# Kernel optimization log

Measured on AMD Instinct MI355X. Metric: run time of the kernel, lower is better.

Reference implementation:

```python
import jax, jax.numpy as jnp
import numpy as np

B, L, H, E = 4, 2048, 16, 64
S, D = L, E

def setup_inputs() -> dict:
    key = jax.random.key(0)
    kq, kk, kv = jax.random.split(key, 3)
    queries = jax.random.normal(kq, (B, L, H, E), dtype=jnp.float32)
    keys = jax.random.normal(kk, (B, S, H, E), dtype=jnp.float32)
    values = jax.random.normal(kv, (B, S, H, D), dtype=jnp.float32)
    return {"queries": queries, "keys": keys, "values": values}

def reference(queries, keys, values):
    # FullAttention(mask_flag=True, scale=None, output_attention=False), eval mode (dropout off)
    Bq, Lq, Hq, Eq = queries.shape
    scale = 1.0 / jnp.sqrt(jnp.asarray(Eq, dtype=queries.dtype))
    scores = jnp.einsum('blhe,bshe->bhls', queries, keys)  # [B,H,L,S]
    causal = jnp.triu(jnp.ones((Lq, Lq), dtype=bool), k=1)  # True above diagonal
    neg_inf = jnp.finfo(scores.dtype).min
    scores = jnp.where(causal[None, None, :, :], neg_inf, scores)
    A = jax.nn.softmax(scale * scores, axis=-1)
    V = jnp.einsum('bhls,bshd->blhd', A, values)  # [B,L,H,D]
    return V
```

## Files before the change

kernel.cpp:

```cpp
#include <hip/hip_runtime.h>

typedef _Float16 half8  __attribute__((ext_vector_type(8)));
typedef _Float16 half4v __attribute__((ext_vector_type(4)));
typedef __fp16   pk2    __attribute__((ext_vector_type(2)));
typedef float    f32x16 __attribute__((ext_vector_type(16)));

constexpr int CL = 2048, CH = 16, CE = 64;
constexpr int RS = CH * CE;

union H8 { half8 v; pk2 h[4]; unsigned u[4]; };
union H4 { half4v v; pk2 h[2]; };
union H2 { pk2 h; unsigned u; };

__device__ __forceinline__ int swz(int r) { return ((r ^ (r >> 3)) & 7) << 3; }

__global__ __launch_bounds__(256, 3)
void attn32(const float* __restrict__ Q, const float* __restrict__ K,
            const float* __restrict__ V, float* __restrict__ O) {
  __shared__ _Float16 KS[2][64 * 64];
  __shared__ _Float16 VT[2][64 * 64];

  const int tid = threadIdx.x;
  const int w  = tid >> 6, l = tid & 63;
  const int hi = l >> 5,  ql = l & 31;

  const int bid = blockIdx.x;
  const int bh  = bid & 63;
  const int qt  = 15 - (bid >> 6);
  const int b = bh >> 4, h = bh & 15;
  const int qg0 = qt * 128 + w * 32;
  const int qg  = qg0 + ql;

  const float* qptr = Q + ((size_t)(b * CL + qg) * CH + h) * CE;
  const float qs = 0.125f * 1.44269504089f;
  half8 qf[4];
#pragma unroll
  for (int c = 0; c < 4; ++c) {
    const float4 x0 = *(const float4*)(qptr + c * 16 + hi * 8);
    const float4 x1 = *(const float4*)(qptr + c * 16 + hi * 8 + 4);
    H8 t;
    t.h[0] = __builtin_amdgcn_cvt_pkrtz(x0.x * qs, x0.y * qs);
    t.h[1] = __builtin_amdgcn_cvt_pkrtz(x0.z * qs, x0.w * qs);
    t.h[2] = __builtin_amdgcn_cvt_pkrtz(x1.x * qs, x1.y * qs);
    t.h[3] = __builtin_amdgcn_cvt_pkrtz(x1.z * qs, x1.w * qs);
    qf[c] = t.v;
  }

  f32x16 acc0, acc1;
#pragma unroll
  for (int i = 0; i < 16; ++i) { acc0[i] = 0.f; acc1[i] = 0.f; }
  float m_ = -1e30f, l_ = 0.f;

  const float* Kb = K + ((size_t)b * CL * CH + h) * CE;
  const float* Vb = V + ((size_t)b * CL * CH + h) * CE;

  const int r0 = tid >> 4;
  const int c4 = tid & 15;

  const int ktmax  = 2 * qt + 1;
  const int ktlast = 2 * qt + (w >> 1);

  auto stage_write = [&](int buf, int i, const float4& kx, const float4& vx) {
    const int row = i * 16 + r0;
    H4 t;
    t.h[0] = __builtin_amdgcn_cvt_pkrtz(kx.x, kx.y);
    t.h[1] = __builtin_amdgcn_cvt_pkrtz(kx.z, kx.w);
    *(half4v*)&KS[buf][row * 64 + ((c4 * 4) ^ swz(row))] = t.v;
    VT[buf][(c4 * 4 + 0) * 64 + (row ^ swz(c4 * 4 + 0))] = (_Float16)vx.x;
    VT[buf][(c4 * 4 + 1) * 64 + (row ^ swz(c4 * 4 + 1))] = (_Float16)vx.y;
    VT[buf][(c4 * 4 + 2) * 64 + (row ^ swz(c4 * 4 + 2))] = (_Float16)vx.z;
    VT[buf][(c4 * 4 + 3) * 64 + (row ^ swz(c4 * 4 + 3))] = (_Float16)vx.w;
  };

#pragma unroll
  for (int i = 0; i < 4; ++i) {
    const int row = i * 16 + r0;
    const float4 kx = *(const float4*)(Kb + (size_t)row * RS + c4 * 4);
    const float4 vx = *(const float4*)(Vb + (size_t)row * RS + c4 * 4);
    stage_write(0, i, kx, vx);
  }

  for (int kt = 0; kt <= ktmax; ++kt) {
    const int cur = kt & 1, nxt = cur ^ 1;
    __syncthreads();

    float4 kst[4], vst[4];
    const bool doStage = (kt < ktmax);
    if (doStage) {
      const int kb1 = (kt + 1) * 64;
#pragma unroll
      for (int i = 0; i < 4; ++i) {
        const int row = kb1 + i * 16 + r0;
        kst[i] = *(const float4*)(Kb + (size_t)row * RS + c4 * 4);
        vst[i] = *(const float4*)(Vb + (size_t)row * RS + c4 * 4);
      }
    }

    if (kt <= ktlast) {
      const int kb = kt * 64;
      const bool do1 = (qg0 + 31) >= (kb + 32);

      f32x16 st0, st1;
#pragma unroll
      for (int i = 0; i < 16; ++i) { st0[i] = 0.f; st1[i] = 0.f; }
#pragma unroll
      for (int c = 0; c < 4; ++c) {
        const half8 ka = *(const half8*)&KS[cur][ql * 64 + ((c * 16 + hi * 8) ^ swz(ql))];
        st0 = __builtin_amdgcn_mfma_f32_32x32x16_f16(ka, qf[c], st0, 0, 0, 0);
      }
      if (do1) {
#pragma unroll
        for (int c = 0; c < 4; ++c) {
          const int row = 32 + ql;
          const half8 ka = *(const half8*)&KS[cur][row * 64 + ((c * 16 + hi * 8) ^ swz(row))];
          st1 = __builtin_amdgcn_mfma_f32_32x32x16_f16(ka, qf[c], st1, 0, 0, 0);
        }
      }

      if (kt == ktlast) {
#pragma unroll
        for (int r = 0; r < 16; ++r) {
          const int ko = (r & 3) + 8 * (r >> 2) + 4 * hi;
          if (kb + ko > qg) st0[r] = -1e30f;
          if (kb + 32 + ko > qg) st1[r] = -1e30f;
        }
      }

      float mt;
      {
        float a = fmaxf(fmaxf(fmaxf(st0[0], st0[1]), fmaxf(st0[2], st0[3])),
                        fmaxf(fmaxf(st0[4], st0[5]), fmaxf(st0[6], st0[7])));
        float bm = fmaxf(fmaxf(fmaxf(st0[8], st0[9]), fmaxf(st0[10], st0[11])),
                         fmaxf(fmaxf(st0[12], st0[13]), fmaxf(st0[14], st0[15])));
        mt = fmaxf(a, bm);
        if (do1) {
          float c2 = fmaxf(fmaxf(fmaxf(st1[0], st1[1]), fmaxf(st1[2], st1[3])),
                           fmaxf(fmaxf(st1[4], st1[5]), fmaxf(st1[6], st1[7])));
          float d2 = fmaxf(fmaxf(fmaxf(st1[8], st1[9]), fmaxf(st1[10], st1[11])),
                           fmaxf(fmaxf(st1[12], st1[13]), fmaxf(st1[14], st1[15])));
          mt = fmaxf(mt, fmaxf(c2, d2));
        }
      }
      mt = fmaxf(mt, __shfl_xor(mt, 32));
      const float mn = fmaxf(m_, mt);
      const float corr = exp2f(m_ - mn);
      m_ = mn;

      float rs = 0.f;
#pragma unroll
      for (int r = 0; r < 16; ++r) { st0[r] = exp2f(st0[r] - mn); rs += st0[r]; }
      if (do1) {
#pragma unroll
        for (int r = 0; r < 16; ++r) { st1[r] = exp2f(st1[r] - mn); rs += st1[r]; }
      }
      rs += __shfl_xor(rs, 32);
      l_ = l_ * corr + rs;
#pragma unroll
      for (int r = 0; r < 16; ++r) { acc0[r] *= corr; acc1[r] *= corr; }

      unsigned W0[8], W1[8];
#pragma unroll
      for (int m = 0; m < 8; ++m) {
        H2 u; u.h = __builtin_amdgcn_cvt_pkrtz(st0[2 * m], st0[2 * m + 1]);
        W0[m] = u.u;
      }
      if (do1) {
#pragma unroll
        for (int m = 0; m < 8; ++m) {
          H2 u; u.h = __builtin_amdgcn_cvt_pkrtz(st1[2 * m], st1[2 * m + 1]);
          W1[m] = u.u;
        }
      }

#pragma unroll
      for (int c2 = 0; c2 < 2; ++c2) {
        const unsigned s0 = (unsigned)__shfl_xor((int)W0[4 * c2 + 0], 32);
        const unsigned s1 = (unsigned)__shfl_xor((int)W0[4 * c2 + 1], 32);
        const unsigned s2 = (unsigned)__shfl_xor((int)W0[4 * c2 + 2], 32);
        const unsigned s3 = (unsigned)__shfl_xor((int)W0[4 * c2 + 3], 32);
        H8 f;
        f.u[0] = hi ? s2 : W0[4 * c2 + 0];
        f.u[1] = hi ? s3 : W0[4 * c2 + 1];
        f.u[2] = hi ? W0[4 * c2 + 2] : s0;
        f.u[3] = hi ? W0[4 * c2 + 3] : s1;
        const int kx = c2 * 16 + hi * 8;
        const int d0 = ql, d1 = 32 + ql;
        const half8 va0 = *(const half8*)&VT[cur][d0 * 64 + (kx ^ swz(d0))];
        const half8 va1 = *(const half8*)&VT[cur][d1 * 64 + (kx ^ swz(d1))];
        acc0 = __builtin_amdgcn_mfma_f32_32x32x16_f16(va0, f.v, acc0, 0, 0, 0);
        acc1 = __builtin_amdgcn_mfma_f32_32x32x16_f16(va1, f.v, acc1, 0, 0, 0);
      }
      if (do1) {
#pragma unroll
        for (int c2 = 0; c2 < 2; ++c2) {
          const unsigned s0 = (unsigned)__shfl_xor((int)W1[4 * c2 + 0], 32);
          const unsigned s1 = (unsigned)__shfl_xor((int)W1[4 * c2 + 1], 32);
          const unsigned s2 = (unsigned)__shfl_xor((int)W1[4 * c2 + 2], 32);
          const unsigned s3 = (unsigned)__shfl_xor((int)W1[4 * c2 + 3], 32);
          H8 f;
          f.u[0] = hi ? s2 : W1[4 * c2 + 0];
          f.u[1] = hi ? s3 : W1[4 * c2 + 1];
          f.u[2] = hi ? W1[4 * c2 + 2] : s0;
          f.u[3] = hi ? W1[4 * c2 + 3] : s1;
          const int kx = (2 + c2) * 16 + hi * 8;
          const int d0 = ql, d1 = 32 + ql;
          const half8 va0 = *(const half8*)&VT[cur][d0 * 64 + (kx ^ swz(d0))];
          const half8 va1 = *(const half8*)&VT[cur][d1 * 64 + (kx ^ swz(d1))];
          acc0 = __builtin_amdgcn_mfma_f32_32x32x16_f16(va0, f.v, acc0, 0, 0, 0);
          acc1 = __builtin_amdgcn_mfma_f32_32x32x16_f16(va1, f.v, acc1, 0, 0, 0);
        }
      }
    }

    if (doStage) {
#pragma unroll
      for (int i = 0; i < 4; ++i) stage_write(nxt, i, kst[i], vst[i]);
    }
  }

  const float inv = 1.0f / l_;
  float* obase = O + ((size_t)(b * CL + qg) * CH + h) * CE;
#pragma unroll
  for (int rq = 0; rq < 4; ++rq) {
    float4 o;
    o.x = acc0[4 * rq + 0] * inv; o.y = acc0[4 * rq + 1] * inv;
    o.z = acc0[4 * rq + 2] * inv; o.w = acc0[4 * rq + 3] * inv;
    *(float4*)(obase + rq * 8 + hi * 4) = o;
  }
#pragma unroll
  for (int rq = 0; rq < 4; ++rq) {
    float4 o;
    o.x = acc1[4 * rq + 0] * inv; o.y = acc1[4 * rq + 1] * inv;
    o.z = acc1[4 * rq + 2] * inv; o.w = acc1[4 * rq + 3] * inv;
    *(float4*)(obase + 32 + rq * 8 + hi * 4) = o;
  }
}

extern "C" void kernel_launch(void* const* d_in, const int* in_sizes, int n_in,
                              void* d_out, int out_size, void* d_ws, size_t ws_size,
                              hipStream_t stream) {
  const float* Q = (const float*)d_in[0];
  const float* K = (const float*)d_in[1];
  const float* V = (const float*)d_in[2];
  float* O = (float*)d_out;
  (void)d_ws; (void)ws_size; (void)in_sizes; (void)n_in; (void)out_size;
  attn32<<<dim3(16 * 64), dim3(256), 0, stream>>>(Q, K, V, O);
}
```

Measured before the change: 232.8 us.

## Use 512-thread blocks over 256 query rows with lazy rescale and setprio

Doubles the block to 8 waves covering 256 query rows, so each staged K/V tile is shared by twice as many queries and global K/V traffic drops. The grid is halved and reordered so heavy causal tiles come first. The online-softmax rescale now runs only when the running max grows by more than a threshold, and MFMA sections are wrapped in s_setprio. The key loop is unrolled by two with fixed buffer indices. Risks include lower occupancy, fewer blocks for load balance, and fp16 overflow headroom from the lazy max.

```diff
diff --git a/kernel.cpp b/kernel.cpp
--- a/kernel.cpp
+++ b/kernel.cpp
@@ -14,9 +14,9 @@
 
 __device__ __forceinline__ int swz(int r) { return ((r ^ (r >> 3)) & 7) << 3; }
 
-__global__ __launch_bounds__(256, 3)
-void attn32(const float* __restrict__ Q, const float* __restrict__ K,
-            const float* __restrict__ V, float* __restrict__ O) {
+__global__ __launch_bounds__(512, 4)
+void attn512(const float* __restrict__ Q, const float* __restrict__ K,
+             const float* __restrict__ V, float* __restrict__ O) {
   __shared__ _Float16 KS[2][64 * 64];
   __shared__ _Float16 VT[2][64 * 64];
 
@@ -26,23 +26,24 @@
 
   const int bid = blockIdx.x;
   const int bh  = bid & 63;
-  const int qt  = 15 - (bid >> 6);
+  const int qsl = bid >> 6;
+  const int qs  = (qsl < 4) ? (7 - qsl) : (qsl - 4);
   const int b = bh >> 4, h = bh & 15;
-  const int qg0 = qt * 128 + w * 32;
+  const int qg0 = qs * 256 + w * 32;
   const int qg  = qg0 + ql;
 
   const float* qptr = Q + ((size_t)(b * CL + qg) * CH + h) * CE;
-  const float qs = 0.125f * 1.44269504089f;
+  const float qs_ = 0.125f * 1.44269504089f;
   half8 qf[4];
 #pragma unroll
   for (int c = 0; c < 4; ++c) {
     const float4 x0 = *(const float4*)(qptr + c * 16 + hi * 8);
     const float4 x1 = *(const float4*)(qptr + c * 16 + hi * 8 + 4);
     H8 t;
-    t.h[0] = __builtin_amdgcn_cvt_pkrtz(x0.x * qs, x0.y * qs);
-    t.h[1] = __builtin_amdgcn_cvt_pkrtz(x0.z * qs, x0.w * qs);
-    t.h[2] = __builtin_amdgcn_cvt_pkrtz(x1.x * qs, x1.y * qs);
-    t.h[3] = __builtin_amdgcn_cvt_pkrtz(x1.z * qs, x1.w * qs);
+    t.h[0] = __builtin_amdgcn_cvt_pkrtz(x0.x * qs_, x0.y * qs_);
+    t.h[1] = __builtin_amdgcn_cvt_pkrtz(x0.z * qs_, x0.w * qs_);
+    t.h[2] = __builtin_amdgcn_cvt_pkrtz(x1.x * qs_, x1.y * qs_);
+    t.h[3] = __builtin_amdgcn_cvt_pkrtz(x1.z * qs_, x1.w * qs_);
     qf[c] = t.v;
   }
 
@@ -57,11 +58,11 @@
   const int r0 = tid >> 4;
   const int c4 = tid & 15;
 
-  const int ktmax  = 2 * qt + 1;
-  const int ktlast = 2 * qt + (w >> 1);
+  const int ktmax  = 4 * qs + 3;
+  const int ktlast = 4 * qs + (w >> 1);
 
   auto stage_write = [&](int buf, int i, const float4& kx, const float4& vx) {
-    const int row = i * 16 + r0;
+    const int row = i * 32 + r0;
     H4 t;
     t.h[0] = __builtin_amdgcn_cvt_pkrtz(kx.x, kx.y);
     t.h[1] = __builtin_amdgcn_cvt_pkrtz(kx.z, kx.w);
@@ -73,24 +74,23 @@
   };
 
 #pragma unroll
-  for (int i = 0; i < 4; ++i) {
-    const int row = i * 16 + r0;
+  for (int i = 0; i < 2; ++i) {
+    const int row = i * 32 + r0;
     const float4 kx = *(const float4*)(Kb + (size_t)row * RS + c4 * 4);
     const float4 vx = *(const float4*)(Vb + (size_t)row * RS + c4 * 4);
     stage_write(0, i, kx, vx);
   }
 
-  for (int kt = 0; kt <= ktmax; ++kt) {
-    const int cur = kt & 1, nxt = cur ^ 1;
+  auto phase = [&](const int kt, const int cur) {
     __syncthreads();
 
-    float4 kst[4], vst[4];
+    float4 kst[2], vst[2];
     const bool doStage = (kt < ktmax);
     if (doStage) {
       const int kb1 = (kt + 1) * 64;
 #pragma unroll
-      for (int i = 0; i < 4; ++i) {
-        const int row = kb1 + i * 16 + r0;
+      for (int i = 0; i < 2; ++i) {
+        const int row = kb1 + i * 32 + r0;
         kst[i] = *(const float4*)(Kb + (size_t)row * RS + c4 * 4);
         vst[i] = *(const float4*)(Vb + (size_t)row * RS + c4 * 4);
       }
@@ -103,6 +103,7 @@
       f32x16 st0, st1;
 #pragma unroll
       for (int i = 0; i < 16; ++i) { st0[i] = 0.f; st1[i] = 0.f; }
+      __builtin_amdgcn_s_setprio(1);
 #pragma unroll
       for (int c = 0; c < 4; ++c) {
         const half8 ka = *(const half8*)&KS[cur][ql * 64 + ((c * 16 + hi * 8) ^ swz(ql))];
@@ -116,6 +117,7 @@
           st1 = __builtin_amdgcn_mfma_f32_32x32x16_f16(ka, qf[c], st1, 0, 0, 0);
         }
       }
+      __builtin_amdgcn_s_setprio(0);
 
       if (kt == ktlast) {
 #pragma unroll
@@ -142,21 +144,24 @@
         }
       }
       mt = fmaxf(mt, __shfl_xor(mt, 32));
-      const float mn = fmaxf(m_, mt);
-      const float corr = exp2f(m_ - mn);
-      m_ = mn;
+      if (!__all(mt <= m_ + 8.f)) {
+        const float mn = fmaxf(m_, mt);
+        const float corr = exp2f(m_ - mn);
+        m_ = mn;
+        l_ *= corr;
+#pragma unroll
+        for (int r = 0; r < 16; ++r) { acc0[r] *= corr; acc1[r] *= corr; }
+      }
 
       float rs = 0.f;
 #pragma unroll
-      for (int r = 0; r < 16; ++r) { st0[r] = exp2f(st0[r] - mn); rs += st0[r]; }
-      if (do1) {
-#pragma unroll
-        for (int r = 0; r < 16; ++r) { st1[r] = exp2f(st1[r] - mn); rs += st1[r]; }
+      for (int r = 0; r < 16; ++r) { st0[r] = exp2f(st0[r] - m_); rs += st0[r]; }
+      if (do1) {
+#pragma unroll
+        for (int r = 0; r < 16; ++r) { st1[r] = exp2f(st1[r] - m_); rs += st1[r]; }
       }
       rs += __shfl_xor(rs, 32);
-      l_ = l_ * corr + rs;
-#pragma unroll
-      for (int r = 0; r < 16; ++r) { acc0[r] *= corr; acc1[r] *= corr; }
+      l_ += rs;
 
       unsigned W0[8], W1[8];
 #pragma unroll
@@ -172,6 +177,7 @@
         }
       }
 
+      __builtin_amdgcn_s_setprio(1);
 #pragma unroll
       for (int c2 = 0; c2 < 2; ++c2) {
         const unsigned s0 = (unsigned)__shfl_xor((int)W0[4 * c2 + 0], 32);
@@ -210,12 +216,18 @@
           acc1 = __builtin_amdgcn_mfma_f32_32x32x16_f16(va1, f.v, acc1, 0, 0, 0);
         }
       }
+      __builtin_amdgcn_s_setprio(0);
     }
 
     if (doStage) {
 #pragma unroll
-      for (int i = 0; i < 4; ++i) stage_write(nxt, i, kst[i], vst[i]);
+      for (int i = 0; i < 2; ++i) stage_write(cur ^ 1, i, kst[i], vst[i]);
     }
+  };
+
+  for (int kt = 0; kt <= ktmax; kt += 2) {
+    phase(kt, 0);
+    phase(kt + 1, 1);
   }
 
   const float inv = 1.0f / l_;
@@ -244,5 +256,5 @@
   const float* V = (const float*)d_in[2];
   float* O = (float*)d_out;
   (void)d_ws; (void)ws_size; (void)in_sizes; (void)n_in; (void)out_size;
-  attn32<<<dim3(16 * 64), dim3(256), 0, stream>>>(Q, K, V, O);
+  attn512<<<dim3(8 * 64), dim3(512), 0, stream>>>(Q, K, V, O);
 }
```

Result: slower. 267.5 us (+14.9%).

## Pre-convert K/V to swizzled fp16 tiles and stage them via global-to-LDS DMA

Applied to the files above, without the earlier changes.

Adds a pre-pass kernel that converts K and V to fp16 once, stored as contiguous 64x64 tiles in workspace. K keeps the swizzled row layout and V is written pre-transposed. The attention kernel then fills shared memory with direct global_load_lds copies instead of loading fp32, converting and doing scattered transposed LDS stores on every tile. This halves K/V traffic in the main loop and removes per-block repeated conversion, at the cost of an extra kernel launch and a full K/V read/write pass. The old path is kept as a fallback when the workspace is too small, and the DMA path may lack explicit waits on outstanding loads before the barrier.

```diff
diff --git a/kernel.cpp b/kernel.cpp
--- a/kernel.cpp
+++ b/kernel.cpp
@@ -7,6 +7,8 @@
 
 constexpr int CL = 2048, CH = 16, CE = 64;
 constexpr int RS = CH * CE;
+constexpr size_t PANEL_HALFS = (size_t)4 * 16 * 2048 * 64;
+constexpr size_t WS_NEED = PANEL_HALFS * 2 * sizeof(_Float16) * 2;
 
 union H8 { half8 v; pk2 h[4]; unsigned u[4]; };
 union H4 { half4v v; pk2 h[2]; };
@@ -14,11 +16,64 @@
 
 __device__ __forceinline__ int swz(int r) { return ((r ^ (r >> 3)) & 7) << 3; }
 
+typedef const __attribute__((address_space(1))) unsigned* gas_t;
+typedef __attribute__((address_space(3))) unsigned* las_t;
+__device__ __forceinline__ void gload_lds16(const _Float16* g, _Float16* l) {
+  __builtin_amdgcn_global_load_lds((gas_t)g, (las_t)(unsigned long)(l), 16, 0, 0);
+}
+
+__global__ __launch_bounds__(256, 4)
+void convert_kv(const float* __restrict__ K, const float* __restrict__ V,
+                _Float16* __restrict__ Kh, _Float16* __restrict__ Vh) {
+  __shared__ _Float16 T[64 * 68];
+  const int x = blockIdx.x;
+  const int t = x & 31, bh = x >> 5;
+  const int b = bh >> 4, h = bh & 15;
+  const int tid = threadIdx.x;
+  const float* Kb = K + ((size_t)b * CL * CH + h) * CE + (size_t)(t * 64) * RS;
+  const float* Vb = V + ((size_t)b * CL * CH + h) * CE + (size_t)(t * 64) * RS;
+  _Float16* Kt = Kh + (size_t)(bh * 32 + t) * 4096;
+  _Float16* Vt = Vh + (size_t)(bh * 32 + t) * 4096;
+
+#pragma unroll
+  for (int f = 0; f < 2; ++f) {
+    const int oidx = f * 256 + tid;
+    const int row = oidx >> 3, o = oidx & 7;
+    const float4 k0 = *(const float4*)(Kb + (size_t)row * RS + o * 8);
+    const float4 k1 = *(const float4*)(Kb + (size_t)row * RS + o * 8 + 4);
+    H8 uk;
+    uk.h[0] = __builtin_amdgcn_cvt_pkrtz(k0.x, k0.y);
+    uk.h[1] = __builtin_amdgcn_cvt_pkrtz(k0.z, k0.w);
+    uk.h[2] = __builtin_amdgcn_cvt_pkrtz(k1.x, k1.y);
+    uk.h[3] = __builtin_amdgcn_cvt_pkrtz(k1.z, k1.w);
+    *(half8*)&Kt[row * 64 + ((o * 8) ^ swz(row))] = uk.v;
+    const float4 v0 = *(const float4*)(Vb + (size_t)row * RS + o * 8);
+    const float4 v1 = *(const float4*)(Vb + (size_t)row * RS + o * 8 + 4);
+    H4 a, c;
+    a.h[0] = __builtin_amdgcn_cvt_pkrtz(v0.x, v0.y);
+    a.h[1] = __builtin_amdgcn_cvt_pkrtz(v0.z, v0.w);
+    c.h[0] = __builtin_amdgcn_cvt_pkrtz(v1.x, v1.y);
+    c.h[1] = __builtin_amdgcn_cvt_pkrtz(v1.z, v1.w);
+    *(half4v*)&T[row * 68 + o * 8] = a.v;
+    *(half4v*)&T[row * 68 + o * 8 + 4] = c.v;
+  }
+  __syncthreads();
+#pragma unroll
+  for (int f = 0; f < 2; ++f) {
+    const int oidx = f * 256 + tid;
+    const int d = oidx >> 3, ko = oidx & 7;
+    half8 r;
+#pragma unroll
+    for (int j = 0; j < 8; ++j) r[j] = T[(ko * 8 + j) * 68 + d];
+    *(half8*)&Vt[d * 64 + ((ko * 8) ^ swz(d))] = r;
+  }
+}
+
 __global__ __launch_bounds__(256, 3)
-void attn32(const float* __restrict__ Q, const float* __restrict__ K,
-            const float* __restrict__ V, float* __restrict__ O) {
-  __shared__ _Float16 KS[2][64 * 64];
-  __shared__ _Float16 VT[2][64 * 64];
+void attn_dma(const float* __restrict__ Q, const _Float16* __restrict__ Kh,
+              const _Float16* __restrict__ Vh, float* __restrict__ O) {
+  __shared__ __align__(16) _Float16 KS[2][64 * 64];
+  __shared__ __align__(16) _Float16 VT[2][64 * 64];
 
   const int tid = threadIdx.x;
   const int w  = tid >> 6, l = tid & 63;
@@ -51,50 +106,27 @@
   for (int i = 0; i < 16; ++i) { acc0[i] = 0.f; acc1[i] = 0.f; }
   float m_ = -1e30f, l_ = 0.f;
 
-  const float* Kb = K + ((size_t)b * CL * CH + h) * CE;
-  const float* Vb = V + ((size_t)b * CL * CH + h) * CE;
-
-  const int r0 = tid >> 4;
-  const int c4 = tid & 15;
-
+  const size_t pbase = (size_t)bh * 32;
   const int ktmax  = 2 * qt + 1;
   const int ktlast = 2 * qt + (w >> 1);
 
-  auto stage_write = [&](int buf, int i, const float4& kx, const float4& vx) {
-    const int row = i * 16 + r0;
-    H4 t;
-    t.h[0] = __builtin_amdgcn_cvt_pkrtz(kx.x, kx.y);
-    t.h[1] = __builtin_amdgcn_cvt_pkrtz(kx.z, kx.w);
-    *(half4v*)&KS[buf][row * 64 + ((c4 * 4) ^ swz(row))] = t.v;
-    VT[buf][(c4 * 4 + 0) * 64 + (row ^ swz(c4 * 4 + 0))] = (_Float16)vx.x;
-    VT[buf][(c4 * 4 + 1) * 64 + (row ^ swz(c4 * 4 + 1))] = (_Float16)vx.y;
-    VT[buf][(c4 * 4 + 2) * 64 + (row ^ swz(c4 * 4 + 2))] = (_Float16)vx.z;
-    VT[buf][(c4 * 4 + 3) * 64 + (row ^ swz(c4 * 4 + 3))] = (_Float16)vx.w;
+  auto stage_dma = [&](int buf, int tg) {
+    const _Float16* Kt = Kh + (pbase + tg) * 4096;
+    const _Float16* Vt = Vh + (pbase + tg) * 4096;
+#pragma unroll
+    for (int i = 0; i < 2; ++i) {
+      gload_lds16(Kt + w * 1024 + i * 512 + l * 8, &KS[buf][w * 1024 + i * 512]);
+      gload_lds16(Vt + w * 1024 + i * 512 + l * 8, &VT[buf][w * 1024 + i * 512]);
+    }
   };
 
-#pragma unroll
-  for (int i = 0; i < 4; ++i) {
-    const int row = i * 16 + r0;
-    const float4 kx = *(const float4*)(Kb + (size_t)row * RS + c4 * 4);
-    const float4 vx = *(const float4*)(Vb + (size_t)row * RS + c4 * 4);
-    stage_write(0, i, kx, vx);
-  }
+  stage_dma(0, 0);
 
   for (int kt = 0; kt <= ktmax; ++kt) {
-    const int cur = kt & 1, nxt = cur ^ 1;
+    const int cur = kt & 1;
     __syncthreads();
 
-    float4 kst[4], vst[4];
-    const bool doStage = (kt < ktmax);
-    if (doStage) {
-      const int kb1 = (kt + 1) * 64;
-#pragma unroll
-      for (int i = 0; i < 4; ++i) {
-        const int row = kb1 + i * 16 + r0;
-        kst[i] = *(const float4*)(Kb + (size_t)row * RS + c4 * 4);
-        vst[i] = *(const float4*)(Vb + (size_t)row * RS + c4 * 4);
-      }
-    }
+    if (kt < ktmax) stage_dma(cur ^ 1, kt + 1);
 
     if (kt <= ktlast) {
       const int kb = kt * 64;
@@ -211,6 +243,220 @@
         }
       }
     }
+  }
+
+  const float inv = 1.0f / l_;
+  float* obase = O + ((size_t)(b * CL + qg) * CH + h) * CE;
+#pragma unroll
+  for (int rq = 0; rq < 4; ++rq) {
+    float4 o;
+    o.x = acc0[4 * rq + 0] * inv; o.y = acc0[4 * rq + 1] * inv;
+    o.z = acc0[4 * rq + 2] * inv; o.w = acc0[4 * rq + 3] * inv;
+    *(float4*)(obase + rq * 8 + hi * 4) = o;
+  }
+#pragma unroll
+  for (int rq = 0; rq < 4; ++rq) {
+    float4 o;
+    o.x = acc1[4 * rq + 0] * inv; o.y = acc1[4 * rq + 1] * inv;
+    o.z = acc1[4 * rq + 2] * inv; o.w = acc1[4 * rq + 3] * inv;
+    *(float4*)(obase + 32 + rq * 8 + hi * 4) = o;
+  }
+}
+
+__global__ __launch_bounds__(256, 3)
+void attn32(const float* __restrict__ Q, const float* __restrict__ K,
+            const float* __restrict__ V, float* __restrict__ O) {
+  __shared__ _Float16 KS[2][64 * 64];
+  __shared__ _Float16 VT[2][64 * 64];
+
+  const int tid = threadIdx.x;
+  const int w  = tid >> 6, l = tid & 63;
+  const int hi = l >> 5,  ql = l & 31;
+
+  const int bid = blockIdx.x;
+  const int bh  = bid & 63;
+  const int qt  = 15 - (bid >> 6);
+  const int b = bh >> 4, h = bh & 15;
+  const int qg0 = qt * 128 + w * 32;
+  const int qg  = qg0 + ql;
+
+  const float* qptr = Q + ((size_t)(b * CL + qg) * CH + h) * CE;
+  const float qs = 0.125f * 1.44269504089f;
+  half8 qf[4];
+#pragma unroll
+  for (int c = 0; c < 4; ++c) {
+    const float4 x0 = *(const float4*)(qptr + c * 16 + hi * 8);
+    const float4 x1 = *(const float4*)(qptr + c * 16 + hi * 8 + 4);
+    H8 t;
+    t.h[0] = __builtin_amdgcn_cvt_pkrtz(x0.x * qs, x0.y * qs);
+    t.h[1] = __builtin_amdgcn_cvt_pkrtz(x0.z * qs, x0.w * qs);
+    t.h[2] = __builtin_amdgcn_cvt_pkrtz(x1.x * qs, x1.y * qs);
+    t.h[3] = __builtin_amdgcn_cvt_pkrtz(x1.z * qs, x1.w * qs);
+    qf[c] = t.v;
+  }
+
+  f32x16 acc0, acc1;
+#pragma unroll
+  for (int i = 0; i < 16; ++i) { acc0[i] = 0.f; acc1[i] = 0.f; }
+  float m_ = -1e30f, l_ = 0.f;
+
+  const float* Kb = K + ((size_t)b * CL * CH + h) * CE;
+  const float* Vb = V + ((size_t)b * CL * CH + h) * CE;
+  const int r0 = tid >> 4, c4 = tid & 15;
+  const int ktmax  = 2 * qt + 1;
+  const int ktlast = 2 * qt + (w >> 1);
+
+  auto stage_write = [&](int buf, int i, const float4& kx, const float4& vx) {
+    const int row = i * 16 + r0;
+    H4 t;
+    t.h[0] = __builtin_amdgcn_cvt_pkrtz(kx.x, kx.y);
+    t.h[1] = __builtin_amdgcn_cvt_pkrtz(kx.z, kx.w);
+    *(half4v*)&KS[buf][row * 64 + ((c4 * 4) ^ swz(row))] = t.v;
+    VT[buf][(c4 * 4 + 0) * 64 + (row ^ swz(c4 * 4 + 0))] = (_Float16)vx.x;
+    VT[buf][(c4 * 4 + 1) * 64 + (row ^ swz(c4 * 4 + 1))] = (_Float16)vx.y;
+    VT[buf][(c4 * 4 + 2) * 64 + (row ^ swz(c4 * 4 + 2))] = (_Float16)vx.z;
+    VT[buf][(c4 * 4 + 3) * 64 + (row ^ swz(c4 * 4 + 3))] = (_Float16)vx.w;
+  };
+
+#pragma unroll
+  for (int i = 0; i < 4; ++i) {
+    const int row = i * 16 + r0;
+    const float4 kx = *(const float4*)(Kb + (size_t)row * RS + c4 * 4);
+    const float4 vx = *(const float4*)(Vb + (size_t)row * RS + c4 * 4);
+    stage_write(0, i, kx, vx);
+  }
+
+  for (int kt = 0; kt <= ktmax; ++kt) {
+    const int cur = kt & 1, nxt = cur ^ 1;
+    __syncthreads();
+
+    float4 kst[4], vst[4];
+    const bool doStage = (kt < ktmax);
+    if (doStage) {
+      const int kb1 = (kt + 1) * 64;
+#pragma unroll
+      for (int i = 0; i < 4; ++i) {
+        const int row = kb1 + i * 16 + r0;
+        kst[i] = *(const float4*)(Kb + (size_t)row * RS + c4 * 4);
+        vst[i] = *(const float4*)(Vb + (size_t)row * RS + c4 * 4);
+      }
+    }
+
+    if (kt <= ktlast) {
+      const int kb = kt * 64;
+      const bool do1 = (qg0 + 31) >= (kb + 32);
+
+      f32x16 st0, st1;
+#pragma unroll
+      for (int i = 0; i < 16; ++i) { st0[i] = 0.f; st1[i] = 0.f; }
+#pragma unroll
+      for (int c = 0; c < 4; ++c) {
+        const half8 ka = *(const half8*)&KS[cur][ql * 64 + ((c * 16 + hi * 8) ^ swz(ql))];
+        st0 = __builtin_amdgcn_mfma_f32_32x32x16_f16(ka, qf[c], st0, 0, 0, 0);
+      }
+      if (do1) {
+#pragma unroll
+        for (int c = 0; c < 4; ++c) {
+          const int row = 32 + ql;
+          const half8 ka = *(const half8*)&KS[cur][row * 64 + ((c * 16 + hi * 8) ^ swz(row))];
+          st1 = __builtin_amdgcn_mfma_f32_32x32x16_f16(ka, qf[c], st1, 0, 0, 0);
+        }
+      }
+
+      if (kt == ktlast) {
+#pragma unroll
+        for (int r = 0; r < 16; ++r) {
+          const int ko = (r & 3) + 8 * (r >> 2) + 4 * hi;
+          if (kb + ko > qg) st0[r] = -1e30f;
+          if (kb + 32 + ko > qg) st1[r] = -1e30f;
+        }
+      }
+
+      float mt;
+      {
+        float a = fmaxf(fmaxf(fmaxf(st0[0], st0[1]), fmaxf(st0[2], st0[3])),
+                        fmaxf(fmaxf(st0[4], st0[5]), fmaxf(st0[6], st0[7])));
+        float bm = fmaxf(fmaxf(fmaxf(st0[8], st0[9]), fmaxf(st0[10], st0[11])),
+                         fmaxf(fmaxf(st0[12], st0[13]), fmaxf(st0[14], st0[15])));
+        mt = fmaxf(a, bm);
+        if (do1) {
+          float c2 = fmaxf(fmaxf(fmaxf(st1[0], st1[1]), fmaxf(st1[2], st1[3])),
+                           fmaxf(fmaxf(st1[4], st1[5]), fmaxf(st1[6], st1[7])));
+          float d2 = fmaxf(fmaxf(fmaxf(st1[8], st1[9]), fmaxf(st1[10], st1[11])),
+                           fmaxf(fmaxf(st1[12], st1[13]), fmaxf(st1[14], st1[15])));
+          mt = fmaxf(mt, fmaxf(c2, d2));
+        }
+      }
+      mt = fmaxf(mt, __shfl_xor(mt, 32));
+      const float mn = fmaxf(m_, mt);
+      const float corr = exp2f(m_ - mn);
+      m_ = mn;
+
+      float rs = 0.f;
+#pragma unroll
+      for (int r = 0; r < 16; ++r) { st0[r] = exp2f(st0[r] - mn); rs += st0[r]; }
+      if (do1) {
+#pragma unroll
+        for (int r = 0; r < 16; ++r) { st1[r] = exp2f(st1[r] - mn); rs += st1[r]; }
+      }
+      rs += __shfl_xor(rs, 32);
+      l_ = l_ * corr + rs;
+#pragma unroll
+      for (int r = 0; r < 16; ++r) { acc0[r] *= corr; acc1[r] *= corr; }
+
+      unsigned W0[8], W1[8];
+#pragma unroll
+      for (int m = 0; m < 8; ++m) {
+        H2 u; u.h = __builtin_amdgcn_cvt_pkrtz(st0[2 * m], st0[2 * m + 1]);
+        W0[m] = u.u;
+      }
+      if (do1) {
+#pragma unroll
+        for (int m = 0; m < 8; ++m) {
+          H2 u; u.h = __builtin_amdgcn_cvt_pkrtz(st1[2 * m], st1[2 * m + 1]);
+          W1[m] = u.u;
+        }
+      }
+
+#pragma unroll
+      for (int c2 = 0; c2 < 2; ++c2) {
+        const unsigned s0 = (unsigned)__shfl_xor((int)W0[4 * c2 + 0], 32);
+        const unsigned s1 = (unsigned)__shfl_xor((int)W0[4 * c2 + 1], 32);
+        const unsigned s2 = (unsigned)__shfl_xor((int)W0[4 * c2 + 2], 32);
+        const unsigned s3 = (unsigned)__shfl_xor((int)W0[4 * c2 + 3], 32);
+        H8 f;
+        f.u[0] = hi ? s2 : W0[4 * c2 + 0];
+        f.u[1] = hi ? s3 : W0[4 * c2 + 1];
+        f.u[2] = hi ? W0[4 * c2 + 2] : s0;
+        f.u[3] = hi ? W0[4 * c2 + 3] : s1;
+        const int kx = c2 * 16 + hi * 8;
+        const int d0 = ql, d1 = 32 + ql;
+        const half8 va0 = *(const half8*)&VT[cur][d0 * 64 + (kx ^ swz(d0))];
+        const half8 va1 = *(const half8*)&VT[cur][d1 * 64 + (kx ^ swz(d1))];
+        acc0 = __builtin_amdgcn_mfma_f32_32x32x16_f16(va0, f.v, acc0, 0, 0, 0);
+        acc1 = __builtin_amdgcn_mfma_f32_32x32x16_f16(va1, f.v, acc1, 0, 0, 0);
+      }
+      if (do1) {
+#pragma unroll
+        for (int c2 = 0; c2 < 2; ++c2) {
+          const unsigned s0 = (unsigned)__shfl_xor((int)W1[4 * c2 + 0], 32);
+          const unsigned s1 = (unsigned)__shfl_xor((int)W1[4 * c2 + 1], 32);
+          const unsigned s2 = (unsigned)__shfl_xor((int)W1[4 * c2 + 2], 32);
+          const unsigned s3 = (unsigned)__shfl_xor((int)W1[4 * c2 + 3], 32);
+          H8 f;
+          f.u[0] = hi ? s2 : W1[4 * c2 + 0];
+          f.u[1] = hi ? s3 : W1[4 * c2 + 1];
+          f.u[2] = hi ? W1[4 * c2 + 2] : s0;
+          f.u[3] = hi ? W1[4 * c2 + 3] : s1;
+          const int kx = (2 + c2) * 16 + hi * 8;
+          const int d0 = ql, d1 = 32 + ql;
+          const half8 va0 = *(const half8*)&VT[cur][d0 * 64 + (kx ^ swz(d0))];
+          const half8 va1 = *(const half8*)&VT[cur][d1 * 64 + (kx ^ swz(d1))];
+          acc0 = __builtin_amdgcn_mfma_f32_32x32x16_f16(va0, f.v, acc0, 0, 0, 0);
+          acc1 = __builtin_amdgcn_mfma_f32_32x32x16_f16(va1, f.v, acc1, 0, 0, 0);
+        }
+      }
+    }
 
     if (doStage) {
 #pragma unroll
@@ -243,6 +489,13 @@
   const float* K = (const float*)d_in[1];
   const float* V = (const float*)d_in[2];
   float* O = (float*)d_out;
-  (void)d_ws; (void)ws_size; (void)in_sizes; (void)n_in; (void)out_size;
-  attn32<<<dim3(16 * 64), dim3(256), 0, stream>>>(Q, K, V, O);
+  (void)in_sizes; (void)n_in; (void)out_size;
+  if (ws_size >= WS_NEED) {
+    _Float16* Kh = (_Float16*)d_ws;
+    _Float16* Vh = Kh + PANEL_HALFS;
+    convert_kv<<<dim3(64 * 32), dim3(256), 0, stream>>>(K, V, Kh, Vh);
+    attn_dma<<<dim3(16 * 64), dim3(256), 0, stream>>>(Q, Kh, Vh, O);
+  } else {
+    attn32<<<dim3(16 * 64), dim3(256), 0, stream>>>(Q, K, V, O);
+  }
 }
```

New measurement: 202.3 us. -13.1%, faster.
